# Kernel tuning notes

Measured on AMD Instinct MI355X. Metric: run time of the kernel, lower is better.

## Reference

```python
import jax, jax.numpy as jnp
import numpy as np

B, T, IN, H, L = 512, 1024, 3, 64, 2


def setup_inputs() -> dict:
    key = jax.random.key(0)
    ks = jax.random.split(key, 9)
    k = 1.0 / np.sqrt(H)  # PyTorch GRU init bound
    u = lambda kk, shape: jax.random.uniform(kk, shape, jnp.float32, -k, k)
    x = jax.random.normal(ks[0], (B, T, IN), jnp.float32)
    return {
        "x": x,
        "W_ih0": u(ks[1], (3 * H, IN)), "W_hh0": u(ks[2], (3 * H, H)),
        "b_ih0": u(ks[3], (3 * H,)),   "b_hh0": u(ks[4], (3 * H,)),
        "W_ih1": u(ks[5], (3 * H, H)), "W_hh1": u(ks[6], (3 * H, H)),
        "b_ih1": u(ks[7], (3 * H,)),   "b_hh1": u(ks[8], (3 * H,)),
    }


def _gru_layer(x_tbf, W_ih, W_hh, b_ih, b_hh):
    # x_tbf: [T, B, F]. Precompute input projections for all timesteps (one big GEMM).
    gx = jnp.einsum('tbf,gf->tbg', x_tbf, W_ih) + b_ih  # [T, B, 3H]

    def step(h, gx_t):
        gh = h @ W_hh.T + b_hh  # [B, 3H]
        xr, xz, xn = jnp.split(gx_t, 3, axis=-1)
        hr, hz, hn = jnp.split(gh, 3, axis=-1)
        r = jax.nn.sigmoid(xr + hr)
        z = jax.nn.sigmoid(xz + hz)
        n = jnp.tanh(xn + r * hn)
        h_new = (1.0 - z) * n + z * h
        return h_new, h_new

    h0 = jnp.zeros((x_tbf.shape[1], W_hh.shape[1]), x_tbf.dtype)
    _, ys = jax.lax.scan(step, h0, gx)  # ys: [T, B, H]
    return ys


def reference(x, W_ih0, W_hh0, b_ih0, b_hh0, W_ih1, W_hh1, b_ih1, b_hh1):
    # batch_first input -> time-major for scan
    x_tbf = jnp.swapaxes(x, 0, 1)  # [T, B, IN]
    h1 = _gru_layer(x_tbf, W_ih0, W_hh0, b_ih0, b_hh0)  # [T, B, H]
    h2 = _gru_layer(h1,   W_ih1, W_hh1, b_ih1, b_hh1)  # [T, B, H]
    seq_out = jnp.swapaxes(h2, 0, 1)  # [B, T, H]
    # Dropout is identity in eval mode. h_out[-1] == last-step output of top layer.
    final_hidden = seq_out[:, -1, :]  # [B, H]
    return seq_out, final_hidden
```

## Files before the change

kernel.cpp:

```cpp
#include <hip/hip_runtime.h>


typedef __attribute__((ext_vector_type(8))) short short8;
typedef __attribute__((ext_vector_type(4))) float floatx4;

#define MFMA16(a, b, c) __builtin_amdgcn_mfma_f32_16x16x32_bf16((a), (b), (c), 0, 0, 0)

static constexpr int kB = 512;
static constexpr int kT = 1024;
static constexpr int kIN = 3;
static constexpr int kH = 64;
static constexpr int kBG = 4;
static constexpr int LDH = 72;
static constexpr float kLog2e = 1.44269504f;

__device__ __forceinline__ unsigned short f2bf(float f) {
  unsigned u = __builtin_bit_cast(unsigned, f);
  return (unsigned short)((u + 0x7FFFu + ((u >> 16) & 1u)) >> 16);
}
__device__ __forceinline__ short8 cvt8s(const float* p, float s) {
  short8 f;
#pragma unroll
  for (int j = 0; j < 8; ++j) f[j] = (short)f2bf(p[j] * s);
  return f;
}

#define BLOCK_SYNC() asm volatile("s_waitcnt lgkmcnt(0)\n\ts_barrier" ::: "memory")

__global__ __launch_bounds__(512, 2) void gru_kernel(
    const float* __restrict__ x,
    const float* __restrict__ Wih0, const float* __restrict__ Whh0,
    const float* __restrict__ bih0, const float* __restrict__ bhh0,
    const float* __restrict__ Wih1, const float* __restrict__ Whh1,
    const float* __restrict__ bih1, const float* __restrict__ bhh1,
    float* __restrict__ out) {
  const int tid  = threadIdx.x;
  const int lane = tid & 63;
  const int jt   = (tid >> 6) & 3;
  const int lyr  = tid >> 8;
  const int c    = lane & 15;
  const int grp  = lane >> 4;
  const int wb   = blockIdx.x * kBG;

  __shared__ unsigned short h0buf[2][16 * LDH];
  __shared__ unsigned short h1buf[2][16 * LDH];

  {
    unsigned short* z0 = &h0buf[0][0];
    unsigned short* z1 = &h1buf[0][0];
    for (int i = tid; i < 2 * 16 * LDH; i += 512) { z0[i] = 0; z1[i] = 0; }
  }
  __syncthreads();

  const int gr = jt * 16 + c, gz = 64 + gr, gn = 128 + gr;
  const float gsc[3] = {-kLog2e, -kLog2e, 2.0f * kLog2e};
  const int myrow = grp * 4;

  if (lyr == 0) {
    short8 whh0[2][3], wx[3];
#pragma unroll
    for (int g = 0; g < 3; ++g) {
      const int off = ((g * 4 + jt) * 16 + c) * kH + grp * 8;
      whh0[0][g] = cvt8s(Whh0 + off, gsc[g]);
      whh0[1][g] = cvt8s(Whh0 + off + 32, gsc[g]);
      short8 f = {0, 0, 0, 0, 0, 0, 0, 0};
      if (grp == 0) {
        const float* p = Wih0 + ((g * 4 + jt) * 16 + c) * kIN;
        f[0] = (short)f2bf(p[0] * gsc[g]);
        f[1] = (short)f2bf(p[1] * gsc[g]);
        f[2] = (short)f2bf(p[2] * gsc[g]);
      }
      wx[g] = f;
    }
    const float b0r  = -kLog2e * (bih0[gr] + bhh0[gr]);
    const float b0z  = -kLog2e * (bih0[gz] + bhh0[gz]);
    const float b0nx = 2.0f * kLog2e * bih0[gn];
    const float b0nh = 2.0f * kLog2e * bhh0[gn];

    float h0D = 0.f;
    short8 h0A0 = {0, 0, 0, 0, 0, 0, 0, 0}, h0A1 = h0A0;

    auto load_x = [&](int t) -> short8 {
      short8 f = {0, 0, 0, 0, 0, 0, 0, 0};
      if (grp == 0 && (c & 3) == 0) {
        const float* p = x + ((size_t)(wb + (c >> 2)) * kT + t) * kIN;
        f[0] = (short)f2bf(p[0]); f[1] = (short)f2bf(p[1]); f[2] = (short)f2bf(p[2]);
      }
      return f;
    };
    short8 xf = load_x(0);

#pragma unroll 1
    for (int t = 0; t <= kT; ++t) {
      if (t < kT) {
        floatx4 pr = {b0r, b0r, b0r, b0r};
        pr = MFMA16(xf, wx[0], pr);
        pr = MFMA16(h0A0, whh0[0][0], pr);
        floatx4 qr = {0.f, 0.f, 0.f, 0.f};
        qr = MFMA16(h0A1, whh0[1][0], qr);

        floatx4 pz = {b0z, b0z, b0z, b0z};
        pz = MFMA16(xf, wx[1], pz);
        pz = MFMA16(h0A0, whh0[0][1], pz);
        floatx4 qz = {0.f, 0.f, 0.f, 0.f};
        qz = MFMA16(h0A1, whh0[1][1], qz);

        floatx4 px = {b0nx, b0nx, b0nx, b0nx};
        px = MFMA16(xf, wx[2], px);
        floatx4 ph = {b0nh, b0nh, b0nh, b0nh};
        ph = MFMA16(h0A0, whh0[0][2], ph);
        ph = MFMA16(h0A1, whh0[1][2], ph);

        short8 xn = load_x(t + 1 < kT ? t + 1 : t);

        const float ar  = pr[0] + qr[0];
        const float az  = pz[0] + qz[0];
        const float anx = px[0];
        const float anh = ph[0];
        float rg = __builtin_amdgcn_rcpf(1.0f + __builtin_amdgcn_exp2f(ar));
        float zg = __builtin_amdgcn_rcpf(1.0f + __builtin_amdgcn_exp2f(az));
        float u  = __builtin_amdgcn_rcpf(1.0f + __builtin_amdgcn_exp2f(anx + rg * anh));
        float ng = 1.0f - 2.0f * u;
        float hn = ng + zg * (h0D - ng);
        h0D = hn;
        h0buf[t & 1][myrow * LDH + jt * 16 + c] = f2bf(hn);
        xf = xn;
      }
      BLOCK_SYNC();
      if (t < kT - 1) {
        const unsigned short* s = h0buf[t & 1];
        h0A0 = *(const short8*)(s + c * LDH + grp * 8);
        h0A1 = *(const short8*)(s + c * LDH + 32 + grp * 8);
      }
    }
  } else {
    short8 wih1[2][3], whh1[2][3];
#pragma unroll
    for (int g = 0; g < 3; ++g) {
      const int off = ((g * 4 + jt) * 16 + c) * kH + grp * 8;
      wih1[0][g] = cvt8s(Wih1 + off, gsc[g]);
      wih1[1][g] = cvt8s(Wih1 + off + 32, gsc[g]);
      whh1[0][g] = cvt8s(Whh1 + off, gsc[g]);
      whh1[1][g] = cvt8s(Whh1 + off + 32, gsc[g]);
    }
    const float b1r  = -kLog2e * (bih1[gr] + bhh1[gr]);
    const float b1z  = -kLog2e * (bih1[gz] + bhh1[gz]);
    const float b1nx = 2.0f * kLog2e * bih1[gn];
    const float b1nh = 2.0f * kLog2e * bhh1[gn];

    float h1D = 0.f;
    short8 h1A0 = {0, 0, 0, 0, 0, 0, 0, 0}, h1A1 = h1A0;

    const size_t FH = (size_t)kB * kT * kH;
    float* obase = out + (size_t)(wb + grp) * kT * kH + jt * 16 + c;

#pragma unroll 1
    for (int t = 0; t <= kT; ++t) {
      if (t >= 1) {
        const unsigned short* s0 = h0buf[(t - 1) & 1];
        short8 x0 = *(const short8*)(s0 + c * LDH + grp * 8);
        short8 x1 = *(const short8*)(s0 + c * LDH + 32 + grp * 8);

        floatx4 pr = {b1r, b1r, b1r, b1r};
        pr = MFMA16(h1A0, whh1[0][0], pr);
        pr = MFMA16(h1A1, whh1[1][0], pr);
        floatx4 pz = {b1z, b1z, b1z, b1z};
        pz = MFMA16(h1A0, whh1[0][1], pz);
        pz = MFMA16(h1A1, whh1[1][1], pz);
        floatx4 pnh = {b1nh, b1nh, b1nh, b1nh};
        pnh = MFMA16(h1A0, whh1[0][2], pnh);
        pnh = MFMA16(h1A1, whh1[1][2], pnh);

        floatx4 qr = {0.f, 0.f, 0.f, 0.f};
        qr = MFMA16(x0, wih1[0][0], qr);
        qr = MFMA16(x1, wih1[1][0], qr);
        floatx4 qz = {0.f, 0.f, 0.f, 0.f};
        qz = MFMA16(x0, wih1[0][1], qz);
        qz = MFMA16(x1, wih1[1][1], qz);
        floatx4 qnx = {b1nx, b1nx, b1nx, b1nx};
        qnx = MFMA16(x0, wih1[0][2], qnx);
        qnx = MFMA16(x1, wih1[1][2], qnx);

        const float ar  = pr[0] + qr[0];
        const float az  = pz[0] + qz[0];
        const float anx = qnx[0];
        const float anh = pnh[0];
        float rg = __builtin_amdgcn_rcpf(1.0f + __builtin_amdgcn_exp2f(ar));
        float zg = __builtin_amdgcn_rcpf(1.0f + __builtin_amdgcn_exp2f(az));
        float u  = __builtin_amdgcn_rcpf(1.0f + __builtin_amdgcn_exp2f(anx + rg * anh));
        float ng = 1.0f - 2.0f * u;
        float hn = ng + zg * (h1D - ng);
        h1D = hn;
        h1buf[t & 1][myrow * LDH + jt * 16 + c] = f2bf(hn);

        obase[(size_t)(t - 1) * kH] = hn;
        if (t == kT)
          out[FH + (size_t)(wb + grp) * kH + jt * 16 + c] = hn;
      }
      BLOCK_SYNC();
      if (t >= 1 && t < kT) {
        const unsigned short* s1r = h1buf[t & 1];
        h1A0 = *(const short8*)(s1r + c * LDH + grp * 8);
        h1A1 = *(const short8*)(s1r + c * LDH + 32 + grp * 8);
      }
    }
  }
}

extern "C" void kernel_launch(void* const* d_in, const int* in_sizes, int n_in,
                              void* d_out, int out_size, void* d_ws, size_t ws_size,
                              hipStream_t stream) {
  const float* xp   = (const float*)d_in[0];
  const float* wih0 = (const float*)d_in[1];
  const float* whh0 = (const float*)d_in[2];
  const float* bih0 = (const float*)d_in[3];
  const float* bhh0 = (const float*)d_in[4];
  const float* wih1 = (const float*)d_in[5];
  const float* whh1 = (const float*)d_in[6];
  const float* bih1 = (const float*)d_in[7];
  const float* bhh1 = (const float*)d_in[8];
  float* outp = (float*)d_out;
  hipLaunchKernelGGL(gru_kernel, dim3(kB / kBG), dim3(512), 0, stream,
                     xp, wih0, whh0, bih0, bhh0, wih1, whh1, bih1, bhh1, outp);
}
```

Before: 531.1 us.

## Split GRU layers into separate producer/consumer blocks linked by a global ring buffer

Layer 0 and layer 1 now run in separate 256-thread workgroups (256 blocks) instead of sharing one 512-thread block. Layer 0 publishes bf16 hidden states through a workspace ring buffer with progress flags, and layer 1 spin-waits on those flags. This decouples the two recurrences so each block only syncs its own 4 waves per step. Layer 0's input projection also moves from MFMA to scalar FMAs with x prefetched two steps ahead. The cost is global-memory handoff latency, spin polling, and reliance on all 256 blocks being co-resident to avoid deadlock.

```diff
diff --git a/kernel.cpp b/kernel.cpp
--- a/kernel.cpp
+++ b/kernel.cpp
@@ -3,6 +3,7 @@
 
 typedef __attribute__((ext_vector_type(8))) short short8;
 typedef __attribute__((ext_vector_type(4))) float floatx4;
+typedef __attribute__((ext_vector_type(4))) unsigned uintx4;
 
 #define MFMA16(a, b, c) __builtin_amdgcn_mfma_f32_16x16x32_bf16((a), (b), (c), 0, 0, 0)
 
@@ -10,9 +11,8 @@
 static constexpr int kT = 1024;
 static constexpr int kIN = 3;
 static constexpr int kH = 64;
-static constexpr int kBG = 4;
 static constexpr int LDH = 72;
-static constexpr float kLog2e = 1.44269504f;
+static constexpr float kL2E = 1.44269504f;
 
 __device__ __forceinline__ unsigned short f2bf(float f) {
   unsigned u = __builtin_bit_cast(unsigned, f);
@@ -27,7 +27,205 @@
 
 #define BLOCK_SYNC() asm volatile("s_waitcnt lgkmcnt(0)\n\ts_barrier" ::: "memory")
 
-__global__ __launch_bounds__(512, 2) void gru_kernel(
+__global__ __launch_bounds__(256, 1) void gru_pipe(
+    const float* __restrict__ x,
+    const float* __restrict__ Wih0, const float* __restrict__ Whh0,
+    const float* __restrict__ bih0, const float* __restrict__ bhh0,
+    const float* __restrict__ Wih1, const float* __restrict__ Whh1,
+    const float* __restrict__ bih1, const float* __restrict__ bhh1,
+    float* __restrict__ out, unsigned* __restrict__ flags,
+    unsigned* __restrict__ ring, int D) {
+  const int tid  = threadIdx.x;
+  const int lane = tid & 63;
+  const int jt   = tid >> 6;
+  const int c    = lane & 15;
+  const int grp  = lane >> 4;
+  const int f    = jt * 16 + c;
+  const bool isL1 = blockIdx.x >= 128;
+  const int pair = isL1 ? (int)blockIdx.x - 128 : (int)blockIdx.x;
+  const int b    = pair * 4 + grp;
+  const bool wrap = (D < kT);
+
+  unsigned* prog0 = flags + pair * 32;
+  unsigned* prog1 = flags + pair * 32 + 16;
+  unsigned* rbase = ring + (size_t)pair * D * 128;
+
+  __shared__ __align__(16) unsigned short lds[2][16 * LDH];
+  {
+    unsigned short* z = &lds[0][0];
+    for (int i = tid; i < 2 * 16 * LDH; i += 256) z[i] = 0;
+  }
+  __syncthreads();
+
+  const float gsc[3] = {-kL2E, -kL2E, 2.0f * kL2E};
+  const floatx4 Z = {0.f, 0.f, 0.f, 0.f};
+
+  if (!isL1) {
+    short8 wh[3][2];
+    float wx[3][3];
+#pragma unroll
+    for (int g = 0; g < 3; ++g) {
+      const int row = g * 64 + f;
+      wh[g][0] = cvt8s(Whh0 + row * 64 + grp * 8, gsc[g]);
+      wh[g][1] = cvt8s(Whh0 + row * 64 + 32 + grp * 8, gsc[g]);
+#pragma unroll
+      for (int i = 0; i < 3; ++i) wx[g][i] = Wih0[row * 3 + i] * gsc[g];
+    }
+    const float br  = gsc[0] * (bih0[f] + bhh0[f]);
+    const float bz  = gsc[1] * (bih0[64 + f] + bhh0[64 + f]);
+    const float bnx = gsc[2] * bih0[128 + f];
+    const float bnh = gsc[2] * bhh0[128 + f];
+
+    const float* xb = x + (size_t)b * kT * kIN;
+    float cx0 = xb[0], cx1 = xb[1], cx2 = xb[2];
+    float gxr = fmaf(wx[0][0], cx0, fmaf(wx[0][1], cx1, fmaf(wx[0][2], cx2, br)));
+    float gxz = fmaf(wx[1][0], cx0, fmaf(wx[1][1], cx1, fmaf(wx[1][2], cx2, bz)));
+    float gxn = fmaf(wx[2][0], cx0, fmaf(wx[2][1], cx1, fmaf(wx[2][2], cx2, bnx)));
+    float nx0 = xb[3], nx1 = xb[4], nx2 = xb[5];
+
+    short8 a0 = {0, 0, 0, 0, 0, 0, 0, 0}, a1 = a0;
+    float hp = 0.f;
+    unsigned cons = 0;
+
+#pragma unroll 1
+    for (int t = 0; t < kT; ++t) {
+      floatx4 pr = MFMA16(a0, wh[0][0], Z); pr = MFMA16(a1, wh[0][1], pr);
+      floatx4 pz = MFMA16(a0, wh[1][0], Z); pz = MFMA16(a1, wh[1][1], pz);
+      floatx4 pn = MFMA16(a0, wh[2][0], Z); pn = MFMA16(a1, wh[2][1], pn);
+
+      const float ar = pr[0] + gxr;
+      const float az = pz[0] + gxz;
+      float r_ = __builtin_amdgcn_rcpf(1.0f + __builtin_amdgcn_exp2f(ar));
+      float z_ = __builtin_amdgcn_rcpf(1.0f + __builtin_amdgcn_exp2f(az));
+      float u  = __builtin_amdgcn_rcpf(1.0f + __builtin_amdgcn_exp2f(gxn + r_ * (pn[0] + bnh)));
+      float ng = 1.0f - 2.0f * u;
+      float hn = ng + z_ * (hp - ng);
+      hp = hn;
+
+      const unsigned hb = f2bf(hn);
+      lds[t & 1][(4 * grp) * LDH + f] = (unsigned short)hb;
+
+      if (wrap && t >= D) {
+        while (cons + (unsigned)D < (unsigned)t + 1u)
+          cons = __hip_atomic_load(prog1, __ATOMIC_RELAXED, __HIP_MEMORY_SCOPE_AGENT);
+      }
+      const unsigned ov = (unsigned)__shfl_xor((int)hb, 1);
+      if ((c & 1) == 0)
+        __hip_atomic_store(rbase + (size_t)(t & (D - 1)) * 128 + grp * 32 + jt * 8 + (c >> 1),
+                           hb | (ov << 16), __ATOMIC_RELAXED, __HIP_MEMORY_SCOPE_AGENT);
+
+      gxr = fmaf(wx[0][0], nx0, fmaf(wx[0][1], nx1, fmaf(wx[0][2], nx2, br)));
+      gxz = fmaf(wx[1][0], nx0, fmaf(wx[1][1], nx1, fmaf(wx[1][2], nx2, bz)));
+      gxn = fmaf(wx[2][0], nx0, fmaf(wx[2][1], nx1, fmaf(wx[2][2], nx2, bnx)));
+      if (t + 2 < kT) {
+        const float* p = xb + (size_t)(t + 2) * kIN;
+        nx0 = p[0]; nx1 = p[1]; nx2 = p[2];
+      }
+
+      const bool pub = ((t & 7) == 7) || (t == kT - 1);
+      if (pub) asm volatile("s_waitcnt vmcnt(0)" ::: "memory");
+      BLOCK_SYNC();
+      if (pub && tid == 0)
+        __hip_atomic_store(prog0, (unsigned)(t + 1), __ATOMIC_RELAXED, __HIP_MEMORY_SCOPE_AGENT);
+
+      if (t + 1 < kT) {
+        const unsigned short* s = &lds[t & 1][0];
+        a0 = *(const short8*)(s + c * LDH + grp * 8);
+        a1 = *(const short8*)(s + c * LDH + 32 + grp * 8);
+      }
+    }
+  } else {
+    short8 wi[3][2], wh[3][2];
+#pragma unroll
+    for (int g = 0; g < 3; ++g) {
+      const int row = g * 64 + f;
+      wi[g][0] = cvt8s(Wih1 + row * 64 + grp * 8, gsc[g]);
+      wi[g][1] = cvt8s(Wih1 + row * 64 + 32 + grp * 8, gsc[g]);
+      wh[g][0] = cvt8s(Whh1 + row * 64 + grp * 8, gsc[g]);
+      wh[g][1] = cvt8s(Whh1 + row * 64 + 32 + grp * 8, gsc[g]);
+    }
+    const float b1r  = gsc[0] * (bih1[f] + bhh1[f]);
+    const float b1z  = gsc[1] * (bih1[64 + f] + bhh1[64 + f]);
+    const float b1nx = gsc[2] * bih1[128 + f];
+    const float b1nh = gsc[2] * bhh1[128 + f];
+
+    const bool act = ((c & 3) == 0);
+    const int bat = c >> 2;
+    short8 zf = {0, 0, 0, 0, 0, 0, 0, 0};
+    short8 cur0 = zf, cur1 = zf, nxt0 = zf, nxt1 = zf;
+    short8 h1a0 = zf, h1a1 = zf;
+    float hp = 0.f;
+    unsigned avail = 0;
+    float* ob = out + (size_t)b * kT * kH + f;
+    const size_t FH = (size_t)kB * kT * kH;
+
+    auto load_slot = [&](int s, short8& o0, short8& o1) {
+      if (act) {
+        const unsigned* dp = rbase + (size_t)(s & (D - 1)) * 128 + bat * 32 + grp * 4;
+        uintx4 w0, w1;
+#pragma unroll
+        for (int j = 0; j < 4; ++j)
+          w0[j] = __hip_atomic_load(dp + j, __ATOMIC_RELAXED, __HIP_MEMORY_SCOPE_AGENT);
+#pragma unroll
+        for (int j = 0; j < 4; ++j)
+          w1[j] = __hip_atomic_load(dp + 16 + j, __ATOMIC_RELAXED, __HIP_MEMORY_SCOPE_AGENT);
+        o0 = __builtin_bit_cast(short8, w0);
+        o1 = __builtin_bit_cast(short8, w1);
+      }
+    };
+
+    while (avail < 1u)
+      avail = __hip_atomic_load(prog0, __ATOMIC_RELAXED, __HIP_MEMORY_SCOPE_AGENT);
+    load_slot(0, cur0, cur1);
+
+#pragma unroll 1
+    for (int t = 0; t < kT; ++t) {
+      floatx4 qr = MFMA16(cur0, wi[0][0], Z); qr = MFMA16(cur1, wi[0][1], qr);
+      floatx4 qz = MFMA16(cur0, wi[1][0], Z); qz = MFMA16(cur1, wi[1][1], qz);
+      floatx4 qn = MFMA16(cur0, wi[2][0], Z); qn = MFMA16(cur1, wi[2][1], qn);
+      floatx4 pr = MFMA16(h1a0, wh[0][0], Z); pr = MFMA16(h1a1, wh[0][1], pr);
+      floatx4 pz = MFMA16(h1a0, wh[1][0], Z); pz = MFMA16(h1a1, wh[1][1], pz);
+      floatx4 pn = MFMA16(h1a0, wh[2][0], Z); pn = MFMA16(h1a1, wh[2][1], pn);
+
+      if (t + 1 < kT) {
+        if (avail < (unsigned)t + 2u) {
+          do {
+            avail = __hip_atomic_load(prog0, __ATOMIC_RELAXED, __HIP_MEMORY_SCOPE_AGENT);
+          } while (avail < (unsigned)t + 2u);
+        }
+        load_slot(t + 1, nxt0, nxt1);
+      }
+
+      const float ar = pr[0] + qr[0] + b1r;
+      const float az = pz[0] + qz[0] + b1z;
+      float r_ = __builtin_amdgcn_rcpf(1.0f + __builtin_amdgcn_exp2f(ar));
+      float z_ = __builtin_amdgcn_rcpf(1.0f + __builtin_amdgcn_exp2f(az));
+      float u  = __builtin_amdgcn_rcpf(1.0f + __builtin_amdgcn_exp2f(qn[0] + b1nx + r_ * (pn[0] + b1nh)));
+      float ng = 1.0f - 2.0f * u;
+      float hn = ng + z_ * (hp - ng);
+      hp = hn;
+
+      ob[(size_t)t * kH] = hn;
+      if (t == kT - 1) out[FH + (size_t)b * kH + f] = hn;
+
+      lds[t & 1][(4 * grp) * LDH + f] = f2bf(hn);
+
+      if (wrap && (t & 7) == 7) asm volatile("s_waitcnt vmcnt(0)" ::: "memory");
+      BLOCK_SYNC();
+      if (wrap && (t & 7) == 7 && tid == 0)
+        __hip_atomic_store(prog1, (unsigned)t, __ATOMIC_RELAXED, __HIP_MEMORY_SCOPE_AGENT);
+
+      if (t + 1 < kT) {
+        const unsigned short* s = &lds[t & 1][0];
+        h1a0 = *(const short8*)(s + c * LDH + grp * 8);
+        h1a1 = *(const short8*)(s + c * LDH + 32 + grp * 8);
+        cur0 = nxt0; cur1 = nxt1;
+      }
+    }
+  }
+}
+
+__global__ __launch_bounds__(512, 2) void gru_small(
     const float* __restrict__ x,
     const float* __restrict__ Wih0, const float* __restrict__ Whh0,
     const float* __restrict__ bih0, const float* __restrict__ bhh0,
@@ -40,11 +238,10 @@
   const int lyr  = tid >> 8;
   const int c    = lane & 15;
   const int grp  = lane >> 4;
-  const int wb   = blockIdx.x * kBG;
+  const int wb   = blockIdx.x * 4;
 
   __shared__ unsigned short h0buf[2][16 * LDH];
   __shared__ unsigned short h1buf[2][16 * LDH];
-
   {
     unsigned short* z0 = &h0buf[0][0];
     unsigned short* z1 = &h1buf[0][0];
@@ -53,40 +250,40 @@
   __syncthreads();
 
   const int gr = jt * 16 + c, gz = 64 + gr, gn = 128 + gr;
-  const float gsc[3] = {-kLog2e, -kLog2e, 2.0f * kLog2e};
+  const float gsc[3] = {-kL2E, -kL2E, 2.0f * kL2E};
   const int myrow = grp * 4;
 
   if (lyr == 0) {
-    short8 whh0[2][3], wx[3];
+    short8 whh0[2][3], wxm[3];
 #pragma unroll
     for (int g = 0; g < 3; ++g) {
       const int off = ((g * 4 + jt) * 16 + c) * kH + grp * 8;
       whh0[0][g] = cvt8s(Whh0 + off, gsc[g]);
       whh0[1][g] = cvt8s(Whh0 + off + 32, gsc[g]);
-      short8 f = {0, 0, 0, 0, 0, 0, 0, 0};
+      short8 fv = {0, 0, 0, 0, 0, 0, 0, 0};
       if (grp == 0) {
         const float* p = Wih0 + ((g * 4 + jt) * 16 + c) * kIN;
-        f[0] = (short)f2bf(p[0] * gsc[g]);
-        f[1] = (short)f2bf(p[1] * gsc[g]);
-        f[2] = (short)f2bf(p[2] * gsc[g]);
-      }
-      wx[g] = f;
-    }
-    const float b0r  = -kLog2e * (bih0[gr] + bhh0[gr]);
-    const float b0z  = -kLog2e * (bih0[gz] + bhh0[gz]);
-    const float b0nx = 2.0f * kLog2e * bih0[gn];
-    const float b0nh = 2.0f * kLog2e * bhh0[gn];
+        fv[0] = (short)f2bf(p[0] * gsc[g]);
+        fv[1] = (short)f2bf(p[1] * gsc[g]);
+        fv[2] = (short)f2bf(p[2] * gsc[g]);
+      }
+      wxm[g] = fv;
+    }
+    const float b0r  = gsc[0] * (bih0[gr] + bhh0[gr]);
+    const float b0z  = gsc[1] * (bih0[gz] + bhh0[gz]);
+    const float b0nx = gsc[2] * bih0[gn];
+    const float b0nh = gsc[2] * bhh0[gn];
 
     float h0D = 0.f;
     short8 h0A0 = {0, 0, 0, 0, 0, 0, 0, 0}, h0A1 = h0A0;
 
     auto load_x = [&](int t) -> short8 {
-      short8 f = {0, 0, 0, 0, 0, 0, 0, 0};
+      short8 fv = {0, 0, 0, 0, 0, 0, 0, 0};
       if (grp == 0 && (c & 3) == 0) {
         const float* p = x + ((size_t)(wb + (c >> 2)) * kT + t) * kIN;
-        f[0] = (short)f2bf(p[0]); f[1] = (short)f2bf(p[1]); f[2] = (short)f2bf(p[2]);
-      }
-      return f;
+        fv[0] = (short)f2bf(p[0]); fv[1] = (short)f2bf(p[1]); fv[2] = (short)f2bf(p[2]);
+      }
+      return fv;
     };
     short8 xf = load_x(0);
 
@@ -94,34 +291,29 @@
     for (int t = 0; t <= kT; ++t) {
       if (t < kT) {
         floatx4 pr = {b0r, b0r, b0r, b0r};
-        pr = MFMA16(xf, wx[0], pr);
+        pr = MFMA16(xf, wxm[0], pr);
         pr = MFMA16(h0A0, whh0[0][0], pr);
         floatx4 qr = {0.f, 0.f, 0.f, 0.f};
         qr = MFMA16(h0A1, whh0[1][0], qr);
-
         floatx4 pz = {b0z, b0z, b0z, b0z};
-        pz = MFMA16(xf, wx[1], pz);
+        pz = MFMA16(xf, wxm[1], pz);
         pz = MFMA16(h0A0, whh0[0][1], pz);
         floatx4 qz = {0.f, 0.f, 0.f, 0.f};
         qz = MFMA16(h0A1, whh0[1][1], qz);
-
         floatx4 px = {b0nx, b0nx, b0nx, b0nx};
-        px = MFMA16(xf, wx[2], px);
+        px = MFMA16(xf, wxm[2], px);
         floatx4 ph = {b0nh, b0nh, b0nh, b0nh};
         ph = MFMA16(h0A0, whh0[0][2], ph);
         ph = MFMA16(h0A1, whh0[1][2], ph);
 
         short8 xn = load_x(t + 1 < kT ? t + 1 : t);
 
-        const float ar  = pr[0] + qr[0];
-        const float az  = pz[0] + qz[0];
-        const float anx = px[0];
-        const float anh = ph[0];
-        float rg = __builtin_amdgcn_rcpf(1.0f + __builtin_amdgcn_exp2f(ar));
-        float zg = __builtin_amdgcn_rcpf(1.0f + __builtin_amdgcn_exp2f(az));
-        float u  = __builtin_amdgcn_rcpf(1.0f + __builtin_amdgcn_exp2f(anx + rg * anh));
+        const float ar = pr[0] + qr[0], az = pz[0] + qz[0];
+        float r_ = __builtin_amdgcn_rcpf(1.0f + __builtin_amdgcn_exp2f(ar));
+        float z_ = __builtin_amdgcn_rcpf(1.0f + __builtin_amdgcn_exp2f(az));
+        float u  = __builtin_amdgcn_rcpf(1.0f + __builtin_amdgcn_exp2f(px[0] + r_ * ph[0]));
         float ng = 1.0f - 2.0f * u;
-        float hn = ng + zg * (h0D - ng);
+        float hn = ng + z_ * (h0D - ng);
         h0D = hn;
         h0buf[t & 1][myrow * LDH + jt * 16 + c] = f2bf(hn);
         xf = xn;
@@ -143,10 +335,10 @@
       whh1[0][g] = cvt8s(Whh1 + off, gsc[g]);
       whh1[1][g] = cvt8s(Whh1 + off + 32, gsc[g]);
     }
-    const float b1r  = -kLog2e * (bih1[gr] + bhh1[gr]);
-    const float b1z  = -kLog2e * (bih1[gz] + bhh1[gz]);
-    const float b1nx = 2.0f * kLog2e * bih1[gn];
-    const float b1nh = 2.0f * kLog2e * bhh1[gn];
+    const float b1r  = gsc[0] * (bih1[gr] + bhh1[gr]);
+    const float b1z  = gsc[1] * (bih1[gz] + bhh1[gz]);
+    const float b1nx = gsc[2] * bih1[gn];
+    const float b1nh = gsc[2] * bhh1[gn];
 
     float h1D = 0.f;
     short8 h1A0 = {0, 0, 0, 0, 0, 0, 0, 0}, h1A1 = h1A0;
@@ -181,21 +373,17 @@
         qnx = MFMA16(x0, wih1[0][2], qnx);
         qnx = MFMA16(x1, wih1[1][2], qnx);
 
-        const float ar  = pr[0] + qr[0];
-        const float az  = pz[0] + qz[0];
-        const float anx = qnx[0];
-        const float anh = pnh[0];
-        float rg = __builtin_amdgcn_rcpf(1.0f + __builtin_amdgcn_exp2f(ar));
-        float zg = __builtin_amdgcn_rcpf(1.0f + __builtin_amdgcn_exp2f(az));
-        float u  = __builtin_amdgcn_rcpf(1.0f + __builtin_amdgcn_exp2f(anx + rg * anh));
+        const float ar = pr[0] + qr[0], az = pz[0] + qz[0];
+        float r_ = __builtin_amdgcn_rcpf(1.0f + __builtin_amdgcn_exp2f(ar));
+        float z_ = __builtin_amdgcn_rcpf(1.0f + __builtin_amdgcn_exp2f(az));
+        float u  = __builtin_amdgcn_rcpf(1.0f + __builtin_amdgcn_exp2f(qnx[0] + r_ * pnh[0]));
         float ng = 1.0f - 2.0f * u;
-        float hn = ng + zg * (h1D - ng);
+        float hn = ng + z_ * (h1D - ng);
         h1D = hn;
         h1buf[t & 1][myrow * LDH + jt * 16 + c] = f2bf(hn);
 
         obase[(size_t)(t - 1) * kH] = hn;
-        if (t == kT)
-          out[FH + (size_t)(wb + grp) * kH + jt * 16 + c] = hn;
+        if (t == kT) out[FH + (size_t)(wb + grp) * kH + jt * 16 + c] = hn;
       }
       BLOCK_SYNC();
       if (t >= 1 && t < kT) {
@@ -220,6 +408,23 @@
   const float* bih1 = (const float*)d_in[7];
   const float* bhh1 = (const float*)d_in[8];
   float* outp = (float*)d_out;
-  hipLaunchKernelGGL(gru_kernel, dim3(kB / kBG), dim3(512), 0, stream,
-                     xp, wih0, whh0, bih0, bhh0, wih1, whh1, bih1, bhh1, outp);
+
+  const size_t FLAGB = 16384;
+  const size_t perDepth = (size_t)128 * 512;
+  size_t availB = (ws_size > FLAGB) ? ws_size - FLAGB : 0;
+  int maxD = (int)(availB / perDepth);
+
+  if (d_ws != nullptr && maxD >= 8) {
+    int D = 8;
+    while (D * 2 <= maxD && D < kT) D *= 2;
+    hipMemsetAsync(d_ws, 0, FLAGB, stream);
+    unsigned* flags = (unsigned*)d_ws;
+    unsigned* ring  = (unsigned*)((char*)d_ws + FLAGB);
+    hipLaunchKernelGGL(gru_pipe, dim3(256), dim3(256), 0, stream,
+                       xp, wih0, whh0, bih0, bhh0, wih1, whh1, bih1, bhh1,
+                       outp, flags, ring, D);
+  } else {
+    hipLaunchKernelGGL(gru_small, dim3(kB / 4), dim3(512), 0, stream,
+                       xp, wih0, whh0, bih0, bhh0, wih1, whh1, bih1, bhh1, outp);
+  }
 }
```

Result: slower. 997.8 us (+87.9%).
